# Optimization experiments

Hardware: AMD Instinct MI355X
Metric: run time of the kernel (lower is better)

Reference implementation:

```python
import jax, jax.numpy as jnp
import numpy as np

B, N, H, NH = 2, 48, 256, 8
DH = H // NH  # attention head size = 32


def setup_inputs() -> dict:
    key = jax.random.key(0)
    ks = jax.random.split(key, 12)
    s = 0.02
    return {
        "attention_mask": jnp.zeros((B, 1, N, N), jnp.float32),
        "structure_matrix_pair": jax.random.normal(ks[0], (B, N, N, H), jnp.float32),
        "structure_matrix_triplet": jax.random.normal(ks[1], (B, N, N, N, H), jnp.float32),
        # Linear weights stored [in, out] (x @ W + b == torch Linear with W.T)
        "Wq": jax.random.normal(ks[2], (H, H), jnp.float32) * s, "bq": jnp.zeros((H,), jnp.float32),
        "Wk": jax.random.normal(ks[3], (H, H), jnp.float32) * s, "bk": jnp.zeros((H,), jnp.float32),
        "Wv": jax.random.normal(ks[4], (H, H), jnp.float32) * s, "bv": jnp.zeros((H,), jnp.float32),
        "Wsq": jax.random.normal(ks[5], (H, DH), jnp.float32) * s, "bsq": jnp.zeros((DH,), jnp.float32),
        "Wsk": jax.random.normal(ks[6], (H, DH), jnp.float32) * s, "bsk": jnp.zeros((DH,), jnp.float32),
        "Wsv": jax.random.normal(ks[7], (H, DH), jnp.float32) * s, "bsv": jnp.zeros((DH,), jnp.float32),
    }


def reference(attention_mask, structure_matrix_pair, structure_matrix_triplet,
              Wq, bq, Wk, bk, Wv, bv, Wsq, bsq, Wsk, bsk, Wsv, bsv):
    def heads(x):  # [B,N,N,H] -> [B,NH,N,N,DH]
        return x.reshape(B, N, N, NH, DH).transpose(0, 3, 1, 2, 4)

    q = heads(structure_matrix_pair @ Wq + bq)[:, :, :, None, :, :]  # [B,h,N,1,N,dh]
    k = heads(structure_matrix_pair @ Wk + bk)[:, :, :, :, None, :]  # [B,h,N,N,1,dh]
    v = heads(structure_matrix_pair @ Wv + bv)[:, :, :, None, :, :]  # [B,h,N,1,N,dh]

    sq = (structure_matrix_triplet @ Wsq + bsq)[:, None]  # [B,1,N,N,N,dh]
    sk = (structure_matrix_triplet @ Wsk + bsk)[:, None]
    sv = (structure_matrix_triplet @ Wsv + bsv)[:, None]

    q = q + sq  # [B,h,N,N,N,dh]
    k = k + sk
    v = v + sv

    scores = jnp.sum(q * k, axis=-1) / np.sqrt(DH).astype(np.float32)  # [B,h,N,N,N]
    scores = scores + attention_mask[:, :, None, :, :]
    probs = jax.nn.softmax(scores, axis=-1)
    # dropout is identity in eval mode
    ctx = jnp.einsum('bhikj,bhikjd->bhikd', probs, v)  # sum over last N (j)
    # [B,h,N,N,dh] -> [B,N,N,h*dh]
    return ctx.transpose(0, 2, 3, 1, 4).reshape(B, N, N, NH * DH)
```

## Files before the change

kernel.cpp:

```cpp
#include <hip/hip_runtime.h>
#include <hip/hip_bf16.h>

#define B_ 2
#define N_ 48
#define H_ 256
#define NH_ 8
#define DH_ 32
#define SQS_LD 100

typedef __attribute__((ext_vector_type(8))) short bf16x8;
typedef __attribute__((ext_vector_type(4))) float f32x4;

__device__ __forceinline__ unsigned short f2bf(float f) {
  unsigned u = __float_as_uint(f);
  u += 0x7FFFu + ((u >> 16) & 1u);
  return (unsigned short)(u >> 16);
}

__device__ __forceinline__ bf16x8 cvt8(float4 x, float4 y) {
  union { unsigned u[4]; bf16x8 v; } o;
  asm("v_cvt_pk_bf16_f32 %0, %1, %2" : "=v"(o.u[0]) : "v"(x.x), "v"(x.y));
  asm("v_cvt_pk_bf16_f32 %0, %1, %2" : "=v"(o.u[1]) : "v"(x.z), "v"(x.w));
  asm("v_cvt_pk_bf16_f32 %0, %1, %2" : "=v"(o.u[2]) : "v"(y.x), "v"(y.y));
  asm("v_cvt_pk_bf16_f32 %0, %1, %2" : "=v"(o.u[3]) : "v"(y.z), "v"(y.w));
  return o.v;
}

__device__ __forceinline__ void bar_lgkm() {
  asm volatile("s_waitcnt lgkmcnt(0)" ::: "memory");
  __builtin_amdgcn_s_barrier();
  asm volatile("" ::: "memory");
}

__device__ __forceinline__ void stage48x256(const float* __restrict__ src, char* tAc, int tid) {
#pragma unroll
  for (int it = 0; it < 4; ++it) {
    int c = it * 384 + tid;
    const float4* g = reinterpret_cast<const float4*>(src) + (c << 1);
    float4 x = g[0];
    float4 y = g[1];
    int row = c >> 5;
    int off = (row << 9) + ((c & 31) << 4);
    off ^= (row & 7) << 4;
    *reinterpret_cast<bf16x8*>(tAc + off) = cvt8(x, y);
  }
}

__global__ __launch_bounds__(384, 3)
void pair_proj_kernel(const float* __restrict__ pair,
                      const float* __restrict__ Wq, const float* __restrict__ Wk,
                      const float* __restrict__ Wv, const float* __restrict__ bq,
                      const float* __restrict__ bk, const float* __restrict__ bv,
                      const float* __restrict__ Wsq, const float* __restrict__ Wsk,
                      const float* __restrict__ Wsv, const float* __restrict__ bsq,
                      const float* __restrict__ bsk, const float* __restrict__ bsv,
                      unsigned short* __restrict__ qplane, float* __restrict__ kplane,
                      unsigned short* __restrict__ vplane,
                      unsigned short* __restrict__ wfrag_main, float* __restrict__ biasm) {
  __shared__ __align__(16) char tAc[48 * 256 * 2];
  int tid = threadIdx.x;
  int lane = tid & 63;
  int wave = tid >> 6;
  int gm = blockIdx.x >> 3;
  int gn = blockIdx.x & 7;

  stage48x256(pair + (size_t)gm * 12288, tAc, tid);

  int col = gn * 96 + wave * 16 + (lane & 15);
  const float* Wsel = (col < 256) ? Wq : (col < 512) ? Wk : Wv;
  const float* bsel = (col < 256) ? bq : (col < 512) ? bk : bv;
  int cc = col & 255;
  bf16x8 wf[8];
#pragma unroll
  for (int kt = 0; kt < 8; ++kt) {
    int kbase = kt * 32 + ((lane >> 4) << 3);
    float4 w0, w1;
    w0.x = Wsel[(kbase + 0) * 256 + cc];
    w0.y = Wsel[(kbase + 1) * 256 + cc];
    w0.z = Wsel[(kbase + 2) * 256 + cc];
    w0.w = Wsel[(kbase + 3) * 256 + cc];
    w1.x = Wsel[(kbase + 4) * 256 + cc];
    w1.y = Wsel[(kbase + 5) * 256 + cc];
    w1.z = Wsel[(kbase + 6) * 256 + cc];
    w1.w = Wsel[(kbase + 7) * 256 + cc];
    wf[kt] = cvt8(w0, w1);
  }
  float bias = bsel[cc];

  if (gn == 7) {
    if (tid < 256) {
      int p = gm * 256 + tid;
      int i8 = p & 7, l2 = (p >> 3) & 63, kt2 = (p >> 9) & 7, nt2 = p >> 12;
      int k2 = kt2 * 32 + ((l2 >> 4) << 3) + i8;
      int n2 = nt2 * 16 + (l2 & 15);
      const float* W = (n2 < 32) ? Wsq : (n2 < 64) ? Wsk : Wsv;
      wfrag_main[p] = f2bf(W[k2 * 32 + (n2 & 31)]);
    } else if (gm == 0 && tid < 352) {
      int p = tid - 256;
      biasm[p] = (p < 32) ? bsq[p] : (p < 64) ? bsk[p - 32] : bsv[p - 64];
    }
  }
  __syncthreads();

  f32x4 acc[3];
#pragma unroll
  for (int mt = 0; mt < 3; ++mt) acc[mt] = (f32x4){0.f, 0.f, 0.f, 0.f};
#pragma unroll
  for (int kt = 0; kt < 8; ++kt) {
#pragma unroll
    for (int mt = 0; mt < 3; ++mt) {
      int row = mt * 16 + (lane & 15);
      int off = (row << 9) + (kt << 6) + ((lane >> 4) << 4);
      off ^= (row & 7) << 4;
      bf16x8 a = *reinterpret_cast<const bf16x8*>(tAc + off);
      acc[mt] = __builtin_amdgcn_mfma_f32_16x16x32_bf16(a, wf[kt], acc[mt], 0, 0, 0);
    }
  }

  int jb = (lane >> 4) * 4;
#pragma unroll
  for (int mt = 0; mt < 3; ++mt) {
#pragma unroll
    for (int rr = 0; rr < 4; ++rr) {
      int j = mt * 16 + jb + rr;
      size_t row = (size_t)(gm * 48 + j) * 256;
      float val = acc[mt][rr] + bias;
      if (col < 256) qplane[row + col] = f2bf(val);
      else if (col < 512) kplane[row + (col - 256)] = val;
      else vplane[row + (col - 512)] = f2bf(val);
    }
  }
}

__global__ __launch_bounds__(384, 6)
void e2e_fused(const float* __restrict__ mask, const float* __restrict__ trip,
               const unsigned short* __restrict__ qplane, const float* __restrict__ kplane,
               const unsigned short* __restrict__ vplane,
               const unsigned short* __restrict__ wfragm,
               const float* __restrict__ biasm, float* __restrict__ out) {
  __shared__ __align__(16) char smem[48 * 256 * 2];
  __shared__ float khl[256];
  __shared__ float pbuf[8][48];
  char* tAc = smem;
  float* sqS = reinterpret_cast<float*>(smem);

  int tid = threadIdx.x;
  int lane = tid & 63;
  int wave = tid >> 6;

  int bid = blockIdx.x;
  int s = (bid & 7) * 576 + (bid >> 3);
  int g = s / 48;
  int k = s % 48;
  int b = g / 48;
  int rowbase = g * 48;

  if (tid < 256) khl[tid] = kplane[(size_t)s * 256 + tid];

  const float4* src = reinterpret_cast<const float4*>(trip + (size_t)s * 12288);
  int r0 = tid >> 4, c0 = tid & 15;
  int r1 = (384 + tid) >> 4, c1 = tid & 15;
  float4 pa[4], pb[4];
  pa[0] = src[r0 * 64 + c0 * 2];
  pa[1] = src[r0 * 64 + c0 * 2 + 1];
  pa[2] = src[r1 * 64 + c1 * 2];
  pa[3] = src[r1 * 64 + c1 * 2 + 1];
  pb[0] = src[r0 * 64 + 32 + c0 * 2];
  pb[1] = src[r0 * 64 + 32 + c0 * 2 + 1];
  pb[2] = src[r1 * 64 + 32 + c1 * 2];
  pb[3] = src[r1 * 64 + 32 + c1 * 2 + 1];

  {
    int off0 = (r0 << 9) + (c0 << 4);
    off0 ^= (r0 & 7) << 4;
    *reinterpret_cast<bf16x8*>(tAc + off0) = cvt8(pa[0], pa[1]);
    int off1 = (r1 << 9) + (c1 << 4);
    off1 ^= (r1 & 7) << 4;
    *reinterpret_cast<bf16x8*>(tAc + off1) = cvt8(pa[2], pa[3]);
  }
  bar_lgkm();

  const bf16x8* wp = reinterpret_cast<const bf16x8*>(wfragm);
  f32x4 acc[3];
#pragma unroll
  for (int mt = 0; mt < 3; ++mt) acc[mt] = (f32x4){0.f, 0.f, 0.f, 0.f};
#pragma unroll
  for (int kt = 0; kt < 4; ++kt) {
    bf16x8 w = wp[(wave * 8 + kt) * 64 + lane];
#pragma unroll
    for (int mt = 0; mt < 3; ++mt) {
      int row = mt * 16 + (lane & 15);
      int off = (row << 9) + (kt << 6) + ((lane >> 4) << 4);
      off ^= (row & 7) << 4;
      bf16x8 a = *reinterpret_cast<const bf16x8*>(tAc + off);
      acc[mt] = __builtin_amdgcn_mfma_f32_16x16x32_bf16(a, w, acc[mt], 0, 0, 0);
    }
  }
  {
    int off0 = (r0 << 9) + ((16 + c0) << 4);
    off0 ^= (r0 & 7) << 4;
    *reinterpret_cast<bf16x8*>(tAc + off0) = cvt8(pb[0], pb[1]);
    int off1 = (r1 << 9) + ((16 + c1) << 4);
    off1 ^= (r1 & 7) << 4;
    *reinterpret_cast<bf16x8*>(tAc + off1) = cvt8(pb[2], pb[3]);
  }
  bar_lgkm();

#pragma unroll
  for (int kt = 4; kt < 8; ++kt) {
    bf16x8 w = wp[(wave * 8 + kt) * 64 + lane];
#pragma unroll
    for (int mt = 0; mt < 3; ++mt) {
      int row = mt * 16 + (lane & 15);
      int off = (row << 9) + (kt << 6) + ((lane >> 4) << 4);
      off ^= (row & 7) << 4;
      bf16x8 a = *reinterpret_cast<const bf16x8*>(tAc + off);
      acc[mt] = __builtin_amdgcn_mfma_f32_16x16x32_bf16(a, w, acc[mt], 0, 0, 0);
    }
  }
  bar_lgkm();

  {
    int n = wave * 16 + (lane & 15);
    float bias = biasm[n];
    int jb = (lane >> 4) * 4;
#pragma unroll
    for (int mt = 0; mt < 3; ++mt) {
#pragma unroll
      for (int rr = 0; rr < 4; ++rr)
        sqS[(mt * 16 + jb + rr) * SQS_LD + n] = acc[mt][rr] + bias;
    }
  }
  bar_lgkm();

  {
    int j = tid % 48, h = tid / 48;
    const uint4* qp = reinterpret_cast<const uint4*>(qplane + (size_t)(rowbase + j) * 256 + h * 32);
    const float4* sq4 = reinterpret_cast<const float4*>(sqS + j * SQS_LD);
    const float4* kh4 = reinterpret_cast<const float4*>(khl + h * 32);
    float sc = 0.f;
#pragma unroll
    for (int q4i = 0; q4i < 4; ++q4i) {
      uint4 qw = qp[q4i];
      float4 sqA = sq4[q4i * 2], sqB = sq4[q4i * 2 + 1];
      float4 skA = sq4[8 + q4i * 2], skB = sq4[8 + q4i * 2 + 1];
      float4 khA = kh4[q4i * 2], khB = kh4[q4i * 2 + 1];
      sc += (__uint_as_float(qw.x << 16) + sqA.x) * (khA.x + skA.x);
      sc += (__uint_as_float(qw.x & 0xFFFF0000u) + sqA.y) * (khA.y + skA.y);
      sc += (__uint_as_float(qw.y << 16) + sqA.z) * (khA.z + skA.z);
      sc += (__uint_as_float(qw.y & 0xFFFF0000u) + sqA.w) * (khA.w + skA.w);
      sc += (__uint_as_float(qw.z << 16) + sqB.x) * (khB.x + skB.x);
      sc += (__uint_as_float(qw.z & 0xFFFF0000u) + sqB.y) * (khB.y + skB.y);
      sc += (__uint_as_float(qw.w << 16) + sqB.z) * (khB.z + skB.z);
      sc += (__uint_as_float(qw.w & 0xFFFF0000u) + sqB.w) * (khB.w + skB.w);
    }
    pbuf[h][j] = sc * 0.17677669529663687f + mask[b * 2304 + k * 48 + j];
  }
  bar_lgkm();

  for (int h = wave; h < 8; h += 6) {
    float x = (lane < 48) ? pbuf[h][lane] : -INFINITY;
    float m = x;
#pragma unroll
    for (int off = 32; off; off >>= 1) m = fmaxf(m, __shfl_xor(m, off));
    float e = (lane < 48) ? __expf(x - m) : 0.f;
    float sum = e;
#pragma unroll
    for (int off = 32; off; off >>= 1) sum += __shfl_xor(sum, off);
    if (lane < 48) pbuf[h][lane] = e / sum;
  }
  bar_lgkm();

  if (tid < 256) {
    int h = tid >> 5, d = tid & 31;
    const unsigned short* vbase = vplane + (size_t)rowbase * 256 + tid;
    float a = 0.f;
#pragma unroll 8
    for (int j = 0; j < 48; ++j) {
      float v = __uint_as_float((unsigned)vbase[(size_t)j * 256] << 16);
      a += pbuf[h][j] * (v + sqS[j * SQS_LD + 64 + d]);
    }
    out[(size_t)s * 256 + tid] = a;
  }
}

extern "C" void kernel_launch(void* const* d_in, const int* in_sizes, int n_in,
                              void* d_out, int out_size, void* d_ws, size_t ws_size,
                              hipStream_t stream) {
  const float* mask = (const float*)d_in[0];
  const float* pair = (const float*)d_in[1];
  const float* trip = (const float*)d_in[2];
  const float* Wq = (const float*)d_in[3];
  const float* bq = (const float*)d_in[4];
  const float* Wk = (const float*)d_in[5];
  const float* bk = (const float*)d_in[6];
  const float* Wv = (const float*)d_in[7];
  const float* bv = (const float*)d_in[8];
  const float* Wsq = (const float*)d_in[9];
  const float* bsq = (const float*)d_in[10];
  const float* Wsk = (const float*)d_in[11];
  const float* bsk = (const float*)d_in[12];
  const float* Wsv = (const float*)d_in[13];
  const float* bsv = (const float*)d_in[14];

  char* ws = (char*)d_ws;
  unsigned short* qplane = (unsigned short*)ws;
  float* kplane = (float*)(ws + 2359296);
  unsigned short* vplane = (unsigned short*)(ws + 7077888);
  unsigned short* wfrag_main = (unsigned short*)(ws + 9437184);
  float* biasm = (float*)(ws + 9486336);

  pair_proj_kernel<<<768, 384, 0, stream>>>(pair, Wq, Wk, Wv, bq, bk, bv,
                                            Wsq, Wsk, Wsv, bsq, bsk, bsv,
                                            qplane, kplane, vplane,
                                            wfrag_main, biasm);
  e2e_fused<<<4608, 384, 0, stream>>>(mask, trip, qplane, kplane, vplane,
                                      wfrag_main, biasm, (float*)d_out);
}
```

Before: 72.48 us.

## Transpose sv into separate LDS buffer and split score dot across lanes with shuffles

The sv projection output now goes to a transposed LDS buffer (svT) with its own padded stride, so the PV loop can read float4 of sv and float4 of probabilities per step. The Q·K score computation changes from one thread per (head, j) doing a 32-wide serial dot to 8 lanes per j, each handling 4 dims across all heads, reduced with xor shuffles. These changes aim to cut LDS bank conflicts and serial dependency chains in the score and context phases. They cost extra shuffle instructions and a little more shared memory, and only 384 threads cover the 48×8 score work.

```diff
diff --git a/kernel.cpp b/kernel.cpp
--- a/kernel.cpp
+++ b/kernel.cpp
@@ -6,7 +6,8 @@
 #define H_ 256
 #define NH_ 8
 #define DH_ 32
-#define SQS_LD 100
+#define SQS_LD 68
+#define SVT_LD 52
 
 typedef __attribute__((ext_vector_type(8))) short bf16x8;
 typedef __attribute__((ext_vector_type(4))) float f32x4;
@@ -139,8 +140,9 @@
                const unsigned short* __restrict__ wfragm,
                const float* __restrict__ biasm, float* __restrict__ out) {
   __shared__ __align__(16) char smem[48 * 256 * 2];
-  __shared__ float khl[256];
-  __shared__ float pbuf[8][48];
+  __shared__ __align__(16) float svT[32 * SVT_LD];
+  __shared__ __align__(16) float khl[256];
+  __shared__ __align__(16) float pbuf[8][48];
   char* tAc = smem;
   float* sqS = reinterpret_cast<float*>(smem);
 
@@ -224,37 +226,51 @@
     int n = wave * 16 + (lane & 15);
     float bias = biasm[n];
     int jb = (lane >> 4) * 4;
-#pragma unroll
-    for (int mt = 0; mt < 3; ++mt) {
-#pragma unroll
-      for (int rr = 0; rr < 4; ++rr)
-        sqS[(mt * 16 + jb + rr) * SQS_LD + n] = acc[mt][rr] + bias;
+    if (wave < 4) {
+#pragma unroll
+      for (int mt = 0; mt < 3; ++mt) {
+#pragma unroll
+        for (int rr = 0; rr < 4; ++rr)
+          sqS[(mt * 16 + jb + rr) * SQS_LD + n] = acc[mt][rr] + bias;
+      }
+    } else {
+      int d = n - 64;
+#pragma unroll
+      for (int mt = 0; mt < 3; ++mt) {
+#pragma unroll
+        for (int rr = 0; rr < 4; ++rr)
+          svT[d * SVT_LD + mt * 16 + jb + rr] = acc[mt][rr] + bias;
+      }
     }
   }
   bar_lgkm();
 
   {
-    int j = tid % 48, h = tid / 48;
-    const uint4* qp = reinterpret_cast<const uint4*>(qplane + (size_t)(rowbase + j) * 256 + h * 32);
-    const float4* sq4 = reinterpret_cast<const float4*>(sqS + j * SQS_LD);
-    const float4* kh4 = reinterpret_cast<const float4*>(khl + h * 32);
-    float sc = 0.f;
-#pragma unroll
-    for (int q4i = 0; q4i < 4; ++q4i) {
-      uint4 qw = qp[q4i];
-      float4 sqA = sq4[q4i * 2], sqB = sq4[q4i * 2 + 1];
-      float4 skA = sq4[8 + q4i * 2], skB = sq4[8 + q4i * 2 + 1];
-      float4 khA = kh4[q4i * 2], khB = kh4[q4i * 2 + 1];
-      sc += (__uint_as_float(qw.x << 16) + sqA.x) * (khA.x + skA.x);
-      sc += (__uint_as_float(qw.x & 0xFFFF0000u) + sqA.y) * (khA.y + skA.y);
-      sc += (__uint_as_float(qw.y << 16) + sqA.z) * (khA.z + skA.z);
-      sc += (__uint_as_float(qw.y & 0xFFFF0000u) + sqA.w) * (khA.w + skA.w);
-      sc += (__uint_as_float(qw.z << 16) + sqB.x) * (khB.x + skB.x);
-      sc += (__uint_as_float(qw.z & 0xFFFF0000u) + sqB.y) * (khB.y + skB.y);
-      sc += (__uint_as_float(qw.w << 16) + sqB.z) * (khB.z + skB.z);
-      sc += (__uint_as_float(qw.w & 0xFFFF0000u) + sqB.w) * (khB.w + skB.w);
-    }
-    pbuf[h][j] = sc * 0.17677669529663687f + mask[b * 2304 + k * 48 + j];
+    int j = tid >> 3, dq = tid & 7;
+    float4 sq = *reinterpret_cast<const float4*>(sqS + j * SQS_LD + dq * 4);
+    float4 sk = *reinterpret_cast<const float4*>(sqS + j * SQS_LD + 32 + dq * 4);
+    const unsigned short* qrow = qplane + (size_t)(rowbase + j) * 256;
+    float val[8];
+#pragma unroll
+    for (int h = 0; h < 8; ++h) {
+      uint2 qw = *reinterpret_cast<const uint2*>(qrow + h * 32 + dq * 4);
+      float4 kh = *reinterpret_cast<const float4*>(khl + h * 32 + dq * 4);
+      float v = (__uint_as_float(qw.x << 16) + sq.x) * (kh.x + sk.x);
+      v += (__uint_as_float(qw.x & 0xFFFF0000u) + sq.y) * (kh.y + sk.y);
+      v += (__uint_as_float(qw.y << 16) + sq.z) * (kh.z + sk.z);
+      v += (__uint_as_float(qw.y & 0xFFFF0000u) + sq.w) * (kh.w + sk.w);
+      val[h] = v;
+    }
+#pragma unroll
+    for (int h = 0; h < 8; ++h) {
+      val[h] += __shfl_xor(val[h], 1);
+      val[h] += __shfl_xor(val[h], 2);
+      val[h] += __shfl_xor(val[h], 4);
+    }
+    float sc = val[0];
+#pragma unroll
+    for (int h = 1; h < 8; ++h) sc = (dq == h) ? val[h] : sc;
+    pbuf[dq][j] = sc * 0.17677669529663687f + mask[b * 2304 + k * 48 + j];
   }
   bar_lgkm();
 
@@ -275,10 +291,18 @@
     int h = tid >> 5, d = tid & 31;
     const unsigned short* vbase = vplane + (size_t)rowbase * 256 + tid;
     float a = 0.f;
-#pragma unroll 8
-    for (int j = 0; j < 48; ++j) {
-      float v = __uint_as_float((unsigned)vbase[(size_t)j * 256] << 16);
-      a += pbuf[h][j] * (v + sqS[j * SQS_LD + 64 + d]);
+#pragma unroll
+    for (int j4 = 0; j4 < 12; ++j4) {
+      float4 p4 = *reinterpret_cast<const float4*>(&pbuf[h][j4 * 4]);
+      float4 sv4 = *reinterpret_cast<const float4*>(svT + d * SVT_LD + j4 * 4);
+      float v0 = __uint_as_float((unsigned)vbase[(size_t)(j4 * 4 + 0) * 256] << 16);
+      float v1 = __uint_as_float((unsigned)vbase[(size_t)(j4 * 4 + 1) * 256] << 16);
+      float v2 = __uint_as_float((unsigned)vbase[(size_t)(j4 * 4 + 2) * 256] << 16);
+      float v3 = __uint_as_float((unsigned)vbase[(size_t)(j4 * 4 + 3) * 256] << 16);
+      a += p4.x * (v0 + sv4.x);
+      a += p4.y * (v1 + sv4.y);
+      a += p4.z * (v2 + sv4.z);
+      a += p4.w * (v3 + sv4.w);
     }
     out[(size_t)s * 256 + tid] = a;
   }
```

Measured after the change: 72.30 us. Within noise of the previous version (-0.2%).
